# Kernel optimization log

Hardware: AMD Instinct MI355X
Metric: run time of the kernel (lower is better)

Reference implementation:

```python
import jax, jax.numpy as jnp
import numpy as np

T, H, N, Q, C = 65536, 768, 32768, 32768, 10
MAX_LEN = 16  # max span length


def _make_spans(key, n):
    k1, k2 = jax.random.split(key)
    starts = jax.random.randint(k1, (n,), 0, T - MAX_LEN)
    lengths = jax.random.randint(k2, (n,), 1, MAX_LEN + 1)
    return jnp.stack([starts, starts + lengths], axis=1)  # [start, end)


def setup_inputs() -> dict:
    key = jax.random.key(0)
    ks = jax.random.split(key, 6)
    token_emb = jax.random.normal(ks[0], (T, H), dtype=jnp.float32)
    spans_support = _make_spans(ks[1], N)
    labels = jax.random.randint(ks[2], (N,), 0, C)
    spans_query = _make_spans(ks[3], Q)
    W_proj = jax.random.normal(ks[4], (3 * H, H), dtype=jnp.float32) * (1.0 / np.sqrt(3 * H))
    b_proj = jnp.zeros((H,), dtype=jnp.float32)
    return dict(token_emb=token_emb, spans_support=spans_support, labels=labels,
                spans_query=spans_query, W_proj=W_proj, b_proj=b_proj, n_classes=C)


def _span_embed(token_emb, spans, W, b):
    # token_emb: (T, H); spans: (n, 2) [start, end)
    s = spans[:, 0]
    e = spans[:, 1]
    # exclusive-prefix-sum trick turns per-span mean pooling into two gathers
    zero = jnp.zeros((1, token_emb.shape[1]), token_emb.dtype)
    csum = jnp.concatenate([zero, jnp.cumsum(token_emb, axis=0)], axis=0)  # (T+1, H)
    h_mean = (csum[e] - csum[s]) / (e - s).astype(token_emb.dtype)[:, None]
    feat = jnp.concatenate([token_emb[s], token_emb[e - 1], h_mean], axis=-1)  # (n, 3H)
    return jax.nn.gelu(feat @ W + b, approximate=False)  # torch nn.GELU default = erf


def _l2norm(x, eps=1e-12):
    # matches torch F.normalize: x / max(||x||, eps)
    return x / jnp.maximum(jnp.linalg.norm(x, axis=-1, keepdims=True), eps)


def reference(token_emb, spans_support, labels, spans_query, W_proj, b_proj, n_classes):
    sup = _span_embed(token_emb, spans_support, W_proj, b_proj)  # (N, H)
    qry = _span_embed(token_emb, spans_query, W_proj, b_proj)    # (Q, H)
    # prototypes = per-class mean; empty classes fall back to global mean
    sums = jax.ops.segment_sum(sup, labels, num_segments=n_classes)           # (C, H)
    counts = jax.ops.segment_sum(jnp.ones((sup.shape[0],), sup.dtype), labels,
                                 num_segments=n_classes)                       # (C,)
    gmean = sup.mean(axis=0)
    protos = jnp.where(counts[:, None] > 0,
                       sums / jnp.maximum(counts, 1.0)[:, None],
                       gmean[None, :])
    # cosine metric + constant NONE logit of 0.5
    sim = _l2norm(qry) @ _l2norm(protos).T                                     # (Q, C)
    none_logit = jnp.full((qry.shape[0], 1), 0.5, dtype=qry.dtype)
    return jnp.concatenate([sim, none_logit], axis=-1)                         # (Q, C+1)
```

## Files before the change

kernel.cpp:

```cpp
#include <hip/hip_runtime.h>
#include <stdint.h>

#define H_DIM 768
#define N_SUP 32768
#define Q_QRY 32768
#define C_CLS 10
#define M_TOT 65536
#define KG 768
#define NG 2304
#define NT 12
#define NBUCK 1024

typedef __bf16 bf16x8 __attribute__((ext_vector_type(8)));
typedef float f32x4 __attribute__((ext_vector_type(4)));
typedef __attribute__((address_space(3))) void lds_void;
typedef const __attribute__((address_space(1))) void g_void;

__device__ __forceinline__ ushort f2bf(float f) {
  union { float f; uint32_t u; } v; v.f = f;
  uint32_t r = (v.u + 0x7FFFu + ((v.u >> 16) & 1u)) >> 16;
  return (ushort)r;
}
__device__ __forceinline__ float bf2f(ushort h) {
  union { uint32_t u; float f; } v; v.u = ((uint32_t)h) << 16; return v.f;
}
__device__ __forceinline__ float gelu_f(float x) {
  return 0.5f * x * (1.0f + erff(x * 0.70710678118654752f));
}

__global__ void prep_kernel(const float* __restrict__ te, const float* __restrict__ W,
                            const int* __restrict__ spS, const int* __restrict__ spQ,
                            ushort* __restrict__ tb, ushort* __restrict__ Bt,
                            int* __restrict__ histS, int* __restrict__ histQ) {
  int b = blockIdx.x, t = threadIdx.x;
  if (b < 24576) {
    size_t i = (((size_t)b * 256) + t) * 8;
    float4 v0 = *(const float4*)(te + i);
    float4 v1 = *(const float4*)(te + i + 4);
    ushort4 o0, o1;
    o0.x = f2bf(v0.x); o0.y = f2bf(v0.y); o0.z = f2bf(v0.z); o0.w = f2bf(v0.w);
    o1.x = f2bf(v1.x); o1.y = f2bf(v1.y); o1.z = f2bf(v1.z); o1.w = f2bf(v1.w);
    *(ushort4*)(tb + i) = o0;
    *(ushort4*)(tb + i + 4) = o1;
  } else if (b < 31488) {
    int idx = (b - 24576) * 256 + t;
    int n = idx / KG, k = idx - n * KG;
    int blk = n / H_DIM;
    int c = n - blk * H_DIM;
    Bt[idx] = f2bf(W[(size_t)(blk * H_DIM + k) * H_DIM + c]);
  } else {
    __shared__ int lhS[NBUCK], lhQ[NBUCK];
    for (int i = t; i < NBUCK; i += 256) { lhS[i] = 0; lhQ[i] = 0; }
    __syncthreads();
    int b0 = b - 31488;
    for (int i = b0 * 256 + t; i < N_SUP; i += 64 * 256) {
      atomicAdd(&lhS[spS[2 * i] >> 6], 1);
      atomicAdd(&lhQ[spQ[2 * i] >> 6], 1);
    }
    __syncthreads();
    for (int i = t; i < NBUCK; i += 256) {
      if (lhS[i]) atomicAdd(&histS[i], lhS[i]);
      if (lhQ[i]) atomicAdd(&histQ[i], lhQ[i]);
    }
  }
}

__global__ void prefix2_kernel(const int* __restrict__ histS, const int* __restrict__ histQ,
                               int* __restrict__ curS, int* __restrict__ curQ) {
  __shared__ int tmp[NBUCK];
  int t = threadIdx.x;
  {
    int v = histS[t];
    tmp[t] = v;
    __syncthreads();
    for (int off = 1; off < NBUCK; off <<= 1) {
      int add = (t >= off) ? tmp[t - off] : 0;
      __syncthreads();
      tmp[t] += add;
      __syncthreads();
    }
    curS[t] = tmp[t] - v;
    __syncthreads();
  }
  {
    int v = histQ[t];
    tmp[t] = v;
    __syncthreads();
    for (int off = 1; off < NBUCK; off <<= 1) {
      int add = (t >= off) ? tmp[t - off] : 0;
      __syncthreads();
      tmp[t] += add;
      __syncthreads();
    }
    curQ[t] = tmp[t] - v;
  }
}

__global__ void scatter2_kernel(const int* __restrict__ spS, const int* __restrict__ spQ,
                                int* __restrict__ curS, int* __restrict__ curQ,
                                int2* __restrict__ sortedS, int2* __restrict__ sortedQ) {
  for (int i = blockIdx.x * 256 + threadIdx.x; i < N_SUP; i += gridDim.x * 256) {
    {
      int s = spS[2 * i], e = spS[2 * i + 1];
      int pos = atomicAdd(&curS[s >> 6], 1);
      int2 rec; rec.x = s; rec.y = (i << 5) | (e - s);
      sortedS[pos] = rec;
    }
    {
      int s = spQ[2 * i], e = spQ[2 * i + 1];
      int pos = atomicAdd(&curQ[s >> 6], 1);
      int2 rec; rec.x = s; rec.y = (i << 5) | (e - s);
      sortedQ[pos] = rec;
    }
  }
}

__global__ __launch_bounds__(512, 2) void gemm8(const ushort* __restrict__ A,
                                                const ushort* __restrict__ Bt,
                                                ushort* __restrict__ C) {
  __shared__ ushort lds[65536];
  char* ldsc = (char*)lds;

  int orig = blockIdx.x;
  int wg = (orig & 7) * 288 + (orig >> 3);
  int rowT = wg / 9, colT = wg - rowT * 9;
  int m0 = rowT * 256, n0 = colT * 256;

  int tid = threadIdx.x;
  int lane = tid & 63, wave = tid >> 6;
  int wr = wave >> 2, wc = wave & 3;
  int l15 = lane & 15, l4 = lane >> 4;

  int row0 = tid >> 2;
  int ss = (tid & 3) ^ ((row0 >> 1) & 3);
  size_t eA0 = (size_t)(m0 + row0) * KG + ss * 8;
  size_t eA1 = (size_t)(m0 + row0 + 128) * KG + ss * 8;
  size_t eB0 = (size_t)(n0 + row0) * KG + ss * 8;
  size_t eB1 = (size_t)(n0 + row0 + 128) * KG + ss * 8;

  int aoff[8], boff[4];
#pragma unroll
  for (int m = 0; m < 8; ++m) {
    int r = wr * 128 + m * 16 + l15;
    aoff[m] = r * 64 + ((l4 ^ ((r >> 1) & 3)) << 4);
  }
#pragma unroll
  for (int n = 0; n < 4; ++n) {
    int r = wc * 64 + n * 16 + l15;
    boff[n] = r * 64 + ((l4 ^ ((r >> 1) & 3)) << 4);
  }

  f32x4 acc[8][4];
#pragma unroll
  for (int m = 0; m < 8; ++m)
#pragma unroll
    for (int n = 0; n < 4; ++n) acc[m][n] = (f32x4){0.f, 0.f, 0.f, 0.f};

#define SLOT_A(kh, db) (ldsc + ((kh) * 2 + (db)) * 16384)
#define SLOT_B(kh, db) (ldsc + 65536 + ((kh) * 2 + (db)) * 16384)
#define STAGE_A(tk, kh, db) do { \
    char* _d = SLOT_A(kh, db) + wave * 1024; \
    size_t _k = (size_t)(tk) * 64 + (kh) * 32; \
    __builtin_amdgcn_global_load_lds((g_void*)(A + eA0 + _k), (lds_void*)_d, 16, 0, 0); \
    __builtin_amdgcn_global_load_lds((g_void*)(A + eA1 + _k), (lds_void*)(_d + 8192), 16, 0, 0); \
  } while (0)
#define STAGE_B(tk, kh, db) do { \
    char* _d = SLOT_B(kh, db) + wave * 1024; \
    size_t _k = (size_t)(tk) * 64 + (kh) * 32; \
    __builtin_amdgcn_global_load_lds((g_void*)(Bt + eB0 + _k), (lds_void*)_d, 16, 0, 0); \
    __builtin_amdgcn_global_load_lds((g_void*)(Bt + eB1 + _k), (lds_void*)(_d + 8192), 16, 0, 0); \
  } while (0)
#define LDA4(base, o) do { _Pragma("unroll") for (int m = 0; m < 4; ++m) \
    af[m] = *reinterpret_cast<const bf16x8*>((base) + aoff[(o) + m]); } while (0)
#define LDB4(base) do { _Pragma("unroll") for (int n = 0; n < 4; ++n) \
    bf[n] = *reinterpret_cast<const bf16x8*>((base) + boff[n]); } while (0)
#define MFMA_BLOCK(MB) do { _Pragma("unroll") for (int m = 0; m < 4; ++m) \
  _Pragma("unroll") for (int n = 0; n < 4; ++n) \
    acc[(MB) + m][n] = __builtin_amdgcn_mfma_f32_16x16x32_bf16(af[m], bf[n], acc[(MB) + m][n], 0, 0, 0); \
  } while (0)
#define BARX() __builtin_amdgcn_s_barrier()
#define LGKM0() asm volatile("s_waitcnt lgkmcnt(0)" ::: "memory")
#define VM8() asm volatile("s_waitcnt vmcnt(8)" ::: "memory")

  STAGE_A(0, 0, 0); STAGE_B(0, 0, 0);
  STAGE_A(0, 1, 0); STAGE_B(0, 1, 0);
  STAGE_A(1, 0, 1); STAGE_B(1, 0, 1);
  VM8();
  BARX();

  bf16x8 af[4], bf[4];
  for (int t = 0; t < NT; ++t) {
    int d = t & 1, nd = d ^ 1;
    int tk1 = (t + 1 < NT) ? t + 1 : NT - 1;
    int tk2 = (t + 2 < NT) ? t + 2 : NT - 1;
    const char* Ak0 = SLOT_A(0, d); const char* Bk0 = SLOT_B(0, d);
    const char* Ak1 = SLOT_A(1, d); const char* Bk1 = SLOT_B(1, d);
    LDA4(Ak0, 0); LDB4(Bk0);
    STAGE_A(tk1, 1, nd);
    BARX(); LGKM0();
    __builtin_amdgcn_s_setprio(1); MFMA_BLOCK(0); __builtin_amdgcn_s_setprio(0);
    BARX();
    LDA4(Ak0, 4);
    STAGE_B(tk1, 1, nd);
    BARX(); LGKM0();
    __builtin_amdgcn_s_setprio(1); MFMA_BLOCK(4); __builtin_amdgcn_s_setprio(0);
    VM8(); BARX();
    LDA4(Ak1, 0); LDB4(Bk1);
    STAGE_A(tk2, 0, d);
    BARX(); LGKM0();
    __builtin_amdgcn_s_setprio(1); MFMA_BLOCK(0); __builtin_amdgcn_s_setprio(0);
    BARX();
    LDA4(Ak1, 4);
    STAGE_B(tk2, 0, d);
    BARX(); LGKM0();
    __builtin_amdgcn_s_setprio(1); MFMA_BLOCK(4); __builtin_amdgcn_s_setprio(0);
    VM8(); BARX();
  }
  asm volatile("s_waitcnt vmcnt(0)" ::: "memory");

#pragma unroll
  for (int m = 0; m < 8; ++m)
#pragma unroll
    for (int n = 0; n < 4; ++n) {
      int col = n0 + wc * 64 + n * 16 + l15;
      size_t rb = (size_t)(m0 + wr * 128 + m * 16 + l4 * 4) * NG + col;
#pragma unroll
      for (int v = 0; v < 4; ++v)
        C[rb + (size_t)v * NG] = f2bf(acc[m][n][v]);
    }
#undef SLOT_A
#undef SLOT_B
#undef STAGE_A
#undef STAGE_B
#undef LDA4
#undef LDB4
#undef MFMA_BLOCK
}

__device__ __forceinline__ void span_embed(const ushort* __restrict__ PQR,
                                           const float* __restrict__ bias,
                                           int s, int len, int lane, float x[3][4]) {
  int e = s + len;
  float inv = 1.0f / (float)len;
  float acc0[3][4], accr[3][4];
  const ushort* Pr = PQR + (size_t)s * NG;
  const ushort* Qr = PQR + (size_t)(e - 1) * NG + 768;
#pragma unroll
  for (int c = 0; c < 3; ++c) {
    int h = c * 256 + lane * 4;
    ushort4 p = *(const ushort4*)(Pr + h);
    ushort4 q = *(const ushort4*)(Qr + h);
    acc0[c][0] = bf2f(p.x) + bf2f(q.x);
    acc0[c][1] = bf2f(p.y) + bf2f(q.y);
    acc0[c][2] = bf2f(p.z) + bf2f(q.z);
    acc0[c][3] = bf2f(p.w) + bf2f(q.w);
    accr[c][0] = accr[c][1] = accr[c][2] = accr[c][3] = 0.f;
  }
  for (int r = s; r < e; ++r) {
    const ushort* Rr = PQR + (size_t)r * NG + 1536;
#pragma unroll
    for (int c = 0; c < 3; ++c) {
      int h = c * 256 + lane * 4;
      ushort4 rv = *(const ushort4*)(Rr + h);
      accr[c][0] += bf2f(rv.x); accr[c][1] += bf2f(rv.y);
      accr[c][2] += bf2f(rv.z); accr[c][3] += bf2f(rv.w);
    }
  }
#pragma unroll
  for (int c = 0; c < 3; ++c) {
    int h = c * 256 + lane * 4;
    float4 bv = *(const float4*)(bias + h);
    x[c][0] = gelu_f(acc0[c][0] + accr[c][0] * inv + bv.x);
    x[c][1] = gelu_f(acc0[c][1] + accr[c][1] * inv + bv.y);
    x[c][2] = gelu_f(acc0[c][2] + accr[c][2] * inv + bv.z);
    x[c][3] = gelu_f(acc0[c][3] + accr[c][3] * inv + bv.w);
  }
}

__global__ __launch_bounds__(256) void combine_sup(const ushort* __restrict__ PQR,
                                                   const int2* __restrict__ sortedS,
                                                   const int* __restrict__ labels,
                                                   const float* __restrict__ bias,
                                                   float* __restrict__ pSum,
                                                   float* __restrict__ pCnt) {
  __shared__ float ls[C_CLS * H_DIM];
  __shared__ int lc[C_CLS];
  int b = blockIdx.x;
  int sb = ((b & 7) << 5) + (b >> 3);
  int t = threadIdx.x, lane = t & 63, wave = t >> 6;
  for (int i = t; i < C_CLS * H_DIM; i += 256) ls[i] = 0.f;
  if (t < C_CLS) lc[t] = 0;
  __syncthreads();
  for (int k = 0; k < 32; ++k) {
    int wid = sb * 128 + wave * 32 + k;
    int2 rec = sortedS[wid];
    int s = rec.x, len = rec.y & 31, orig = rec.y >> 5;
    float x[3][4];
    span_embed(PQR, bias, s, len, lane, x);
    int lab = labels[orig];
    float* basep = &ls[lab * H_DIM];
#pragma unroll
    for (int c = 0; c < 3; ++c) {
      int h = c * 256 + lane * 4;
      atomicAdd(&basep[h], x[c][0]);
      atomicAdd(&basep[h + 1], x[c][1]);
      atomicAdd(&basep[h + 2], x[c][2]);
      atomicAdd(&basep[h + 3], x[c][3]);
    }
    if (lane == 0) atomicAdd(&lc[lab], 1);
  }
  __syncthreads();
  for (int i = t; i < C_CLS * H_DIM; i += 256) atomicAdd(&pSum[i], ls[i]);
  if (t < C_CLS) atomicAdd(&pCnt[t], (float)lc[t]);
}

__global__ void proto_norm(const float* __restrict__ pSum, const float* __restrict__ pCnt,
                           float* __restrict__ pN) {
  __shared__ float red[4];
  int t = threadIdx.x, lane = t & 63, wave = t >> 6;
  for (int c = 0; c < C_CLS; ++c) {
    float cnt = pCnt[c];
    float x[3];
#pragma unroll
    for (int j = 0; j < 3; ++j) {
      int h = t + j * 256;
      float v;
      if (cnt > 0.5f) v = pSum[c * H_DIM + h] / cnt;
      else {
        float gs = 0.f;
        for (int cc = 0; cc < C_CLS; ++cc) gs += pSum[cc * H_DIM + h];
        v = gs / (float)N_SUP;
      }
      x[j] = v;
    }
    float ss = x[0] * x[0] + x[1] * x[1] + x[2] * x[2];
#pragma unroll
    for (int o = 32; o; o >>= 1) ss += __shfl_xor(ss, o);
    if (lane == 0) red[wave] = ss;
    __syncthreads();
    float tot = red[0] + red[1] + red[2] + red[3];
    float inv = 1.0f / fmaxf(sqrtf(tot), 1e-12f);
#pragma unroll
    for (int j = 0; j < 3; ++j) pN[c * H_DIM + t + j * 256] = x[j] * inv;
    __syncthreads();
  }
}

__global__ __launch_bounds__(256) void combine_qry_sim(const ushort* __restrict__ PQR,
                                                       const int2* __restrict__ sortedQ,
                                                       const float* __restrict__ bias,
                                                       const float* __restrict__ pN,
                                                       float* __restrict__ out) {
  __shared__ float lp[C_CLS * H_DIM];
  int b = blockIdx.x;
  int sb = ((b & 7) << 8) + (b >> 3);
  int t = threadIdx.x, lane = t & 63, wave = t >> 6;
  for (int i = t; i < C_CLS * H_DIM; i += 256) lp[i] = pN[i];
  __syncthreads();
  for (int k = 0; k < 4; ++k) {
    int wid = sb * 16 + wave * 4 + k;
    int2 rec = sortedQ[wid];
    int s = rec.x, len = rec.y & 31, orig = rec.y >> 5;
    float x[3][4];
    span_embed(PQR, bias, s, len, lane, x);
    float sq = 0.f;
    float dot[C_CLS];
#pragma unroll
    for (int p = 0; p < C_CLS; ++p) dot[p] = 0.f;
#pragma unroll
    for (int c = 0; c < 3; ++c) {
      int h = c * 256 + lane * 4;
      sq += x[c][0] * x[c][0] + x[c][1] * x[c][1] + x[c][2] * x[c][2] + x[c][3] * x[c][3];
#pragma unroll
      for (int p = 0; p < C_CLS; ++p) {
        float4 pv = *(const float4*)(lp + p * H_DIM + h);
        dot[p] += x[c][0] * pv.x + x[c][1] * pv.y + x[c][2] * pv.z + x[c][3] * pv.w;
      }
    }
#pragma unroll
    for (int o = 32; o; o >>= 1) {
      sq += __shfl_xor(sq, o);
#pragma unroll
      for (int p = 0; p < C_CLS; ++p) dot[p] += __shfl_xor(dot[p], o);
    }
    if (lane == 0) {
      float inv = 1.0f / fmaxf(sqrtf(sq), 1e-12f);
      float* o = out + (size_t)orig * (C_CLS + 1);
      o[0] = dot[0] * inv; o[1] = dot[1] * inv; o[2] = dot[2] * inv;
      o[3] = dot[3] * inv; o[4] = dot[4] * inv; o[5] = dot[5] * inv;
      o[6] = dot[6] * inv; o[7] = dot[7] * inv; o[8] = dot[8] * inv;
      o[9] = dot[9] * inv; o[10] = 0.5f;
    }
  }
}

extern "C" void kernel_launch(void* const* d_in, const int* in_sizes, int n_in,
                              void* d_out, int out_size, void* d_ws, size_t ws_size,
                              hipStream_t stream) {
  const float* token_emb = (const float*)d_in[0];
  const int*   spansS    = (const int*)d_in[1];
  const int*   labels    = (const int*)d_in[2];
  const int*   spansQ    = (const int*)d_in[3];
  const float* W         = (const float*)d_in[4];
  const float* b         = (const float*)d_in[5];
  float* out = (float*)d_out;

  char* ws = (char*)d_ws;
  size_t pqrB = (size_t)M_TOT * NG * 2;
  size_t tbB  = (size_t)M_TOT * H_DIM * 2;
  size_t wtB  = (size_t)NG * KG * 2;
  ushort* PQR  = (ushort*)ws;
  ushort* tebf = (ushort*)(ws + pqrB);
  ushort* Bt   = (ushort*)(ws + pqrB + tbB);
  char*   tail = ws + pqrB + tbB + wtB;
  float*  pSum = (float*)tail;
  float*  pCnt = pSum + C_CLS * H_DIM;
  float*  pN   = pCnt + 64;
  int*    histS = (int*)(pN + C_CLS * H_DIM);
  int*    histQ = histS + NBUCK;
  int*    curS  = histQ + NBUCK;
  int*    curQ  = curS + NBUCK;
  int2*   sortedS = (int2*)(curQ + NBUCK);
  int2*   sortedQ = sortedS + N_SUP;

  hipMemsetAsync(pSum, 0, (C_CLS * H_DIM + 64) * sizeof(float), stream);
  hipMemsetAsync(histS, 0, 2 * NBUCK * sizeof(int), stream);
  prep_kernel<<<31552, 256, 0, stream>>>(token_emb, W, spansS, spansQ, tebf, Bt, histS, histQ);
  prefix2_kernel<<<1, NBUCK, 0, stream>>>(histS, histQ, curS, curQ);
  scatter2_kernel<<<64, 256, 0, stream>>>(spansS, spansQ, curS, curQ, sortedS, sortedQ);
  gemm8<<<2304, 512, 0, stream>>>(tebf, Bt, PQR);
  combine_sup<<<256, 256, 0, stream>>>(PQR, sortedS, labels, b, pSum, pCnt);
  proto_norm<<<1, 256, 0, stream>>>(pSum, pCnt, pN);
  combine_qry_sim<<<2048, 256, 0, stream>>>(PQR, sortedQ, b, pN, out);
}
```

Before: 674.0 us.

## Split support embedding from prototype accumulation and launch one span per wave

The support combine kernel now writes each span embedding as bf16 into a reused workspace buffer (the bf16 token copy). A new proto_accum kernel then sums those embeddings per class in shared memory without atomics, replacing the many LDS atomics and the low-occupancy 256-block grid. Both combine kernels now launch 8192 blocks with one span per wave, giving more parallelism. The cost is an extra kernel launch, an extra write and read of the support embeddings, and bf16 rounding of the embeddings before they are summed.

Result: faster. 579.9 us (-14.0%).

```diff
diff --git a/kernel.cpp b/kernel.cpp
--- a/kernel.cpp
+++ b/kernel.cpp
@@ -279,35 +279,45 @@
 
 __global__ __launch_bounds__(256) void combine_sup(const ushort* __restrict__ PQR,
                                                    const int2* __restrict__ sortedS,
-                                                   const int* __restrict__ labels,
                                                    const float* __restrict__ bias,
-                                                   float* __restrict__ pSum,
-                                                   float* __restrict__ pCnt) {
+                                                   ushort* __restrict__ embS) {
+  int b = blockIdx.x;
+  int sb = ((b & 7) << 10) + (b >> 3);
+  int wave = threadIdx.x >> 6, lane = threadIdx.x & 63;
+  int wid = sb * 4 + wave;
+  int2 rec = sortedS[wid];
+  int s = rec.x, len = rec.y & 31, orig = rec.y >> 5;
+  float x[3][4];
+  span_embed(PQR, bias, s, len, lane, x);
+  ushort* er = embS + (size_t)orig * H_DIM;
+#pragma unroll
+  for (int c = 0; c < 3; ++c) {
+    int h = c * 256 + lane * 4;
+    ushort4 o;
+    o.x = f2bf(x[c][0]); o.y = f2bf(x[c][1]); o.z = f2bf(x[c][2]); o.w = f2bf(x[c][3]);
+    *(ushort4*)(er + h) = o;
+  }
+}
+
+__global__ void proto_accum(const ushort* __restrict__ supEmb, const int* __restrict__ labels,
+                            float* __restrict__ pSum, float* __restrict__ pCnt) {
   __shared__ float ls[C_CLS * H_DIM];
   __shared__ int lc[C_CLS];
-  int b = blockIdx.x;
-  int sb = ((b & 7) << 5) + (b >> 3);
-  int t = threadIdx.x, lane = t & 63, wave = t >> 6;
+  int t = threadIdx.x;
   for (int i = t; i < C_CLS * H_DIM; i += 256) ls[i] = 0.f;
   if (t < C_CLS) lc[t] = 0;
   __syncthreads();
-  for (int k = 0; k < 32; ++k) {
-    int wid = sb * 128 + wave * 32 + k;
-    int2 rec = sortedS[wid];
-    int s = rec.x, len = rec.y & 31, orig = rec.y >> 5;
-    float x[3][4];
-    span_embed(PQR, bias, s, len, lane, x);
-    int lab = labels[orig];
-    float* basep = &ls[lab * H_DIM];
-#pragma unroll
-    for (int c = 0; c < 3; ++c) {
-      int h = c * 256 + lane * 4;
-      atomicAdd(&basep[h], x[c][0]);
-      atomicAdd(&basep[h + 1], x[c][1]);
-      atomicAdd(&basep[h + 2], x[c][2]);
-      atomicAdd(&basep[h + 3], x[c][3]);
-    }
-    if (lane == 0) atomicAdd(&lc[lab], 1);
+  int base = blockIdx.x * 128;
+  for (int si = 0; si < 128; ++si) {
+    int sp = base + si;
+    int lab = labels[sp];
+    const ushort* er = supEmb + (size_t)sp * H_DIM;
+#pragma unroll
+    for (int j = 0; j < 3; ++j) {
+      int c = t + j * 256;
+      ls[lab * H_DIM + c] += bf2f(er[c]);
+    }
+    if (t == 0) lc[lab]++;
   }
   __syncthreads();
   for (int i = t; i < C_CLS * H_DIM; i += 256) atomicAdd(&pSum[i], ls[i]);
@@ -353,44 +363,42 @@
                                                        float* __restrict__ out) {
   __shared__ float lp[C_CLS * H_DIM];
   int b = blockIdx.x;
-  int sb = ((b & 7) << 8) + (b >> 3);
+  int sb = ((b & 7) << 10) + (b >> 3);
   int t = threadIdx.x, lane = t & 63, wave = t >> 6;
   for (int i = t; i < C_CLS * H_DIM; i += 256) lp[i] = pN[i];
   __syncthreads();
-  for (int k = 0; k < 4; ++k) {
-    int wid = sb * 16 + wave * 4 + k;
-    int2 rec = sortedQ[wid];
-    int s = rec.x, len = rec.y & 31, orig = rec.y >> 5;
-    float x[3][4];
-    span_embed(PQR, bias, s, len, lane, x);
-    float sq = 0.f;
-    float dot[C_CLS];
-#pragma unroll
-    for (int p = 0; p < C_CLS; ++p) dot[p] = 0.f;
-#pragma unroll
-    for (int c = 0; c < 3; ++c) {
-      int h = c * 256 + lane * 4;
-      sq += x[c][0] * x[c][0] + x[c][1] * x[c][1] + x[c][2] * x[c][2] + x[c][3] * x[c][3];
-#pragma unroll
-      for (int p = 0; p < C_CLS; ++p) {
-        float4 pv = *(const float4*)(lp + p * H_DIM + h);
-        dot[p] += x[c][0] * pv.x + x[c][1] * pv.y + x[c][2] * pv.z + x[c][3] * pv.w;
-      }
-    }
-#pragma unroll
-    for (int o = 32; o; o >>= 1) {
-      sq += __shfl_xor(sq, o);
-#pragma unroll
-      for (int p = 0; p < C_CLS; ++p) dot[p] += __shfl_xor(dot[p], o);
-    }
-    if (lane == 0) {
-      float inv = 1.0f / fmaxf(sqrtf(sq), 1e-12f);
-      float* o = out + (size_t)orig * (C_CLS + 1);
-      o[0] = dot[0] * inv; o[1] = dot[1] * inv; o[2] = dot[2] * inv;
-      o[3] = dot[3] * inv; o[4] = dot[4] * inv; o[5] = dot[5] * inv;
-      o[6] = dot[6] * inv; o[7] = dot[7] * inv; o[8] = dot[8] * inv;
-      o[9] = dot[9] * inv; o[10] = 0.5f;
-    }
+  int wid = sb * 4 + wave;
+  int2 rec = sortedQ[wid];
+  int s = rec.x, len = rec.y & 31, orig = rec.y >> 5;
+  float x[3][4];
+  span_embed(PQR, bias, s, len, lane, x);
+  float sq = 0.f;
+  float dot[C_CLS];
+#pragma unroll
+  for (int p = 0; p < C_CLS; ++p) dot[p] = 0.f;
+#pragma unroll
+  for (int c = 0; c < 3; ++c) {
+    int h = c * 256 + lane * 4;
+    sq += x[c][0] * x[c][0] + x[c][1] * x[c][1] + x[c][2] * x[c][2] + x[c][3] * x[c][3];
+#pragma unroll
+    for (int p = 0; p < C_CLS; ++p) {
+      float4 pv = *(const float4*)(lp + p * H_DIM + h);
+      dot[p] += x[c][0] * pv.x + x[c][1] * pv.y + x[c][2] * pv.z + x[c][3] * pv.w;
+    }
+  }
+#pragma unroll
+  for (int o = 32; o; o >>= 1) {
+    sq += __shfl_xor(sq, o);
+#pragma unroll
+    for (int p = 0; p < C_CLS; ++p) dot[p] += __shfl_xor(dot[p], o);
+  }
+  if (lane == 0) {
+    float inv = 1.0f / fmaxf(sqrtf(sq), 1e-12f);
+    float* o = out + (size_t)orig * (C_CLS + 1);
+    o[0] = dot[0] * inv; o[1] = dot[1] * inv; o[2] = dot[2] * inv;
+    o[3] = dot[3] * inv; o[4] = dot[4] * inv; o[5] = dot[5] * inv;
+    o[6] = dot[6] * inv; o[7] = dot[7] * inv; o[8] = dot[8] * inv;
+    o[9] = dot[9] * inv; o[10] = 0.5f;
   }
 }
 
@@ -411,6 +419,7 @@
   size_t wtB  = (size_t)NG * KG * 2;
   ushort* PQR  = (ushort*)ws;
   ushort* tebf = (ushort*)(ws + pqrB);
+  ushort* embS = tebf;
   ushort* Bt   = (ushort*)(ws + pqrB + tbB);
   char*   tail = ws + pqrB + tbB + wtB;
   float*  pSum = (float*)tail;
@@ -429,7 +438,8 @@
   prefix2_kernel<<<1, NBUCK, 0, stream>>>(histS, histQ, curS, curQ);
   scatter2_kernel<<<64, 256, 0, stream>>>(spansS, spansQ, curS, curQ, sortedS, sortedQ);
   gemm8<<<2304, 512, 0, stream>>>(tebf, Bt, PQR);
-  combine_sup<<<256, 256, 0, stream>>>(PQR, sortedS, labels, b, pSum, pCnt);
+  combine_sup<<<8192, 256, 0, stream>>>(PQR, sortedS, b, embS);
+  proto_accum<<<N_SUP / 128, 256, 0, stream>>>(embS, labels, pSum, pCnt);
   proto_norm<<<1, 256, 0, stream>>>(pSum, pCnt, pN);
-  combine_qry_sim<<<2048, 256, 0, stream>>>(PQR, sortedQ, b, pN, out);
-}
+  combine_qry_sim<<<8192, 256, 0, stream>>>(PQR, sortedQ, b, pN, out);
+}
```
